# Kernel optimization log

Hardware: AMD Instinct MI355X
Metric: run time of the kernel (lower is better)

The kernel has to match this reference:

```python
import math
import jax, jax.numpy as jnp
import numpy as np

NUM_HEADS = 32

def _alibi_slopes(n: int) -> jnp.ndarray:
    cp2 = 2 ** int(math.floor(math.log2(n)))
    base = 2.0 ** (-(2.0 ** (-(math.log2(cp2) - 3))))
    slopes = base ** np.arange(1, cp2 + 1, dtype=np.float64)
    if cp2 != n:
        extra_base = 2.0 ** (-(2.0 ** (-(math.log2(2 * cp2) - 3))))
        rem = min(cp2, n - cp2)
        slopes = np.concatenate([slopes, extra_base ** np.arange(1, 1 + 2 * rem, 2, dtype=np.float64)])
    return jnp.asarray(slopes, dtype=jnp.float32)


def setup_inputs() -> dict:
    key = jax.random.key(0)
    k1, k2, k3 = jax.random.split(key, 3)
    B, S, E, H, D = 2, 2048, 4096, NUM_HEADS, 128
    hidden_states = jax.random.normal(k1, (B, S, E), dtype=jnp.float32)
    # torch Linear y = x @ W^T; we store transposed weights [in, out]
    w_qkv = jax.random.normal(k2, (E, H * D + 2 * D), dtype=jnp.float32) * 0.02
    w_c = jax.random.normal(k3, (E, E), dtype=jnp.float32) * 0.02
    return {"hidden_states": hidden_states, "w_qkv": w_qkv, "w_c": w_c}


def reference(hidden_states, w_qkv, w_c):
    B, S, E = hidden_states.shape
    H = NUM_HEADS
    D = E // H
    scaling = D ** -0.5

    qkv = hidden_states @ w_qkv                      # [B,S,H*D+2D]
    q = qkv[..., : H * D].reshape(B, S, H, D)        # [B,S,H,D]
    k = qkv[..., H * D: H * D + D]                   # [B,S,D] single KV head (MQA)
    v = qkv[..., H * D + D:]                         # [B,S,D]

    pos = jnp.arange(S)
    slopes = _alibi_slopes(H)                        # [H]
    # ALiBi: slope * (k_pos - q_pos), <= 0 in the causal region
    bias = slopes[:, None, None] * (pos[None, None, :] - pos[None, :, None]).astype(jnp.float32)  # [H,S,S]

    scores = jnp.einsum('bqhd,bkd->bhqk', q, k) * scaling + bias[None]  # [B,H,S,S]
    causal = pos[:, None] >= pos[None, :]            # [S,S]
    scores = jnp.where(causal[None, None], scores, jnp.finfo(scores.dtype).min)
    probs = jax.nn.softmax(scores, axis=-1)
    attn = jnp.einsum('bhqk,bkd->bqhd', probs, v).reshape(B, S, E)
    return attn @ w_c
```

## Files before the change

kernel.cpp:

```cpp
#include <hip/hip_runtime.h>
#include <hip/hip_bf16.h>

typedef unsigned short u16;
typedef unsigned int u32;
typedef __attribute__((ext_vector_type(8))) short s16x8;
typedef __attribute__((ext_vector_type(4))) float f32x4;

#define MFMA_BF16(a, b, c) __builtin_amdgcn_mfma_f32_16x16x32_bf16(a, b, c, 0, 0, 0)

__device__ __forceinline__ u16 f2bf(float f) {
  union { float f; u32 u; } c; c.f = f;
  return (u16)((c.u + 0x7FFFu + ((c.u >> 16) & 1u)) >> 16);
}

__device__ __forceinline__ u32 pkbf(float a, float b) {
  float2 t; t.x = a; t.y = b;
  __hip_bfloat162 h = __float22bfloat162_rn(t);
  union { __hip_bfloat162 h; u32 u; } c; c.h = h; return c.u;
}

__device__ __forceinline__ void gll16(const void* g, void* l) {
  __builtin_amdgcn_global_load_lds((const __attribute__((address_space(1))) void*)g,
                                   (__attribute__((address_space(3))) void*)l, 16, 0, 0);
}

__device__ __forceinline__ f32x4 f4zero() { f32x4 z = {0.f, 0.f, 0.f, 0.f}; return z; }

__global__ void cvt_bf16_kernel(const float4* __restrict__ in, u16* __restrict__ out, int n4) {
  int i = blockIdx.x * 256 + threadIdx.x;
  if (i >= n4) return;
  float4 v = in[i];
  uint2 w;
  w.x = (u32)f2bf(v.x) | ((u32)f2bf(v.y) << 16);
  w.y = (u32)f2bf(v.z) | ((u32)f2bf(v.w) << 16);
  *reinterpret_cast<uint2*>(out + (size_t)i * 4) = w;
}

__global__ void transpose_cvt_kernel(const float* __restrict__ in, u16* __restrict__ out,
                                     int R, int C) {
  __shared__ float tile[32][33];
  int tx = threadIdx.x, ty = threadIdx.y;
  int r0 = blockIdx.y * 32, c0 = blockIdx.x * 32;
#pragma unroll
  for (int i = 0; i < 32; i += 8)
    tile[ty + i][tx] = in[(size_t)(r0 + ty + i) * C + c0 + tx];
  __syncthreads();
#pragma unroll
  for (int i = 0; i < 32; i += 8)
    out[(size_t)(c0 + ty + i) * R + r0 + tx] = f2bf(tile[tx][ty + i]);
}


#define BARRIER __builtin_amdgcn_s_barrier()
#define LGKM0 asm volatile("s_waitcnt lgkmcnt(0)" ::: "memory")
#define PRIO1 __builtin_amdgcn_s_setprio(1)
#define PRIO0 __builtin_amdgcn_s_setprio(0)
#define VM4 asm volatile("s_waitcnt vmcnt(4)" ::: "memory")
#define VM0 asm volatile("s_waitcnt vmcnt(0)" ::: "memory")
#define NOPSTMT do {} while (0)

#define RD_A(dst, PR, QM) do { _Pragma("unroll")                                         \
  for (int mi2 = 0; mi2 < 4; ++mi2) {                                                    \
    dst[mi2][0] = *(const s16x8*)(smem + (PR)*32768 + (QM)*16384 + mi2*2048 + aOff0);    \
    dst[mi2][1] = *(const s16x8*)(smem + (PR)*32768 + (QM)*16384 + mi2*2048 + aOff1);    \
  } } while (0)

#define RD_B(dst, PR, QN) do { _Pragma("unroll")                                         \
  for (int ni2 = 0; ni2 < 2; ++ni2) {                                                    \
    dst[ni2][0] = *(const s16x8*)(smem + 65536 + (PR)*32768 + (QN)*16384 + ni2*2048 + bOff0); \
    dst[ni2][1] = *(const s16x8*)(smem + 65536 + (PR)*32768 + (QN)*16384 + ni2*2048 + bOff1); \
  } } while (0)

#define MFMA_Q(QM, QN, Af, Bf) do { _Pragma("unroll")                                    \
  for (int ks = 0; ks < 2; ++ks) { _Pragma("unroll")                                     \
    for (int mi2 = 0; mi2 < 4; ++mi2) { _Pragma("unroll")                                \
      for (int ni2 = 0; ni2 < 2; ++ni2)                                                  \
        acc[(QM)*4+mi2][(QN)*2+ni2] =                                                    \
            MFMA_BF16(Af[mi2][ks], Bf[ni2][ks], acc[(QM)*4+mi2][(QN)*2+ni2]);            \
  } } } while (0)

#define STAGE_PAIR(x, PW, kn) do {                                                       \
  gll16(srcA[x] + (kn), smem + (PW)*32768 + (x)*8192 + tt*16);                           \
  gll16(srcB[x] + (kn), smem + 65536 + (PW)*32768 + (x)*8192 + tt*16);                   \
} while (0)

#define STAGE_H1(PW, kn) do { STAGE_PAIR(0, PW, kn); STAGE_PAIR(1, PW, kn); } while (0)
#define STAGE_H2(PW, kn) do { STAGE_PAIR(2, PW, kn); STAGE_PAIR(3, PW, kn); } while (0)

#define TILE_BODY(PR, ST1, ST2, W1, W4) do {                                             \
  s16x8 a0[4][2], a1[4][2], b0[2][2], b1[2][2];                                          \
                       \
  RD_A(a0, PR, 0); RD_B(b0, PR, 0);                                                      \
  ST1;                                                                                   \
  BARRIER; LGKM0; PRIO1; MFMA_Q(0, 0, a0, b0); PRIO0;                                    \
  W1; BARRIER;                                                                           \
                            \
  RD_B(b1, PR, 1);                                                                       \
  ST2;                                                                                   \
  BARRIER; LGKM0; PRIO1; MFMA_Q(0, 1, a0, b1); PRIO0; BARRIER;                           \
                                                    \
  RD_A(a1, PR, 1);                                                                       \
  BARRIER; LGKM0; PRIO1; MFMA_Q(1, 1, a1, b1); PRIO0; BARRIER;                           \
                                                 \
  RD_B(b0, PR, 0);                                                                       \
  BARRIER; LGKM0; PRIO1; MFMA_Q(1, 0, a1, b0); PRIO0;                                    \
  W4; BARRIER;                                                                           \
} while (0)

#define TILE_MAIN(PR, PW, kn) TILE_BODY(PR, STAGE_H1(PW, kn), STAGE_H2(PW, kn), VM4, VM4)
#define TILE_LAST(PR) TILE_BODY(PR, NOPSTMT, NOPSTMT, VM0, NOPSTMT)

template<int EPI>
__global__ __launch_bounds__(512, 2)
void gemm256_kernel(const u16* __restrict__ A, const u16* __restrict__ Bt,
                    float* __restrict__ Cf, u16* __restrict__ Cq,
                    u16* __restrict__ Ck, u16* __restrict__ Cvt,
                    int N, int K) {
  __shared__ __align__(16) char smem[131072];
  const int tt = threadIdx.x;
  const int w = tt >> 6, l = tt & 63;
  const int li = l & 15, g = l >> 4;
  const int wm = w >> 2, wn = w & 3;

  const int gx = gridDim.x;
  const int nwg = gx * gridDim.y;
  int id = blockIdx.y * gx + blockIdx.x;
  id = (id & 7) * (nwg >> 3) + (id >> 3);
  const int bn = id % gx, bm = id / gx;

  f32x4 acc[8][4];
#pragma unroll
  for (int i = 0; i < 8; ++i)
#pragma unroll
    for (int j = 0; j < 4; ++j) acc[i][j] = f4zero();

  const int q8 = (((tt & 7) ^ ((tt >> 3) & 7)) * 8);
  const u16* srcA[4];
  const u16* srcB[4];
#pragma unroll
  for (int x = 0; x < 4; ++x) {
    const int arow = (x & 1) * 128 + (x >> 1) * 64 + (tt >> 3);
    srcA[x] = A + (size_t)(bm * 256 + arow) * K + q8;
    const int rho = x * 64 + (tt >> 3);
    const int qn_ = rho >> 7, rem = rho & 127;
    const int wn_ = rem >> 5, rr = rem & 31;
    const int brow = wn_ * 64 + qn_ * 32 + rr;
    srcB[x] = Bt + (size_t)(bn * 256 + brow) * K + q8;
  }

  const int gr0 = (g ^ (li & 7)) * 16;
  const int aOff0 = wm * 8192 + li * 128 + gr0;
  const int aOff1 = aOff0 ^ 64;
  const int bOff0 = wn * 4096 + li * 128 + gr0;
  const int bOff1 = bOff0 ^ 64;

  STAGE_H1(0, 0);
  STAGE_H2(0, 0);
  VM0;
  BARRIER;

  for (int t2 = 0; t2 < 62; t2 += 2) {
    TILE_MAIN(0, 1, (t2 + 1) * 64);
    TILE_MAIN(1, 0, (t2 + 2) * 64);
  }
  TILE_MAIN(0, 1, 63 * 64);
  TILE_LAST(1);

#pragma unroll
  for (int mi = 0; mi < 8; ++mi) {
#pragma unroll
    for (int ni = 0; ni < 4; ++ni) {
      const int row0 = bm * 256 + wm * 128 + mi * 16 + g * 4;
      const int col = bn * 256 + wn * 64 + ni * 16 + li;
#pragma unroll
      for (int r = 0; r < 4; ++r) {
        const int m = row0 + r;
        const float v = acc[mi][ni][r];
        if (EPI == 0) {
          Cf[(size_t)m * N + col] = v;
        } else {
          const int bb2 = m >> 11, s = m & 2047;
          const int kt = s >> 5;
          const size_t tb = (size_t)(bb2 * 64 + kt);
          if (col < 4096) {
            Cq[(size_t)m * 4096 + col] = f2bf(v);
          } else if (col < 4224) {
            const int d = col - 4096, kr = s & 31;
            const int mk = kr >> 4, lii = kr & 15;
            const int kk = d >> 5, gg = (d >> 3) & 3, e = d & 7;
            Ck[(tb * 8 + mk * 4 + kk) * 512 + (gg * 16 + lii) * 8 + e] = f2bf(v);
          } else {
            const int d = col - 4224, kp = s & 31;
            const int mf = d >> 4, lii = d & 15;
            const int gg = kp >> 3, e = kp & 7;
            Cvt[(tb * 8 + mf) * 512 + (gg * 16 + lii) * 8 + e] = f2bf(v);
          }
        }
      }
    }
  }
}


__device__ __forceinline__ void load_ktile(s16x8 (&dst)[8], const u16* kf, size_t tb, int l) {
#pragma unroll
  for (int f = 0; f < 8; ++f)
    dst[f] = *(const s16x8*)&kf[(tb * 8 + f) * 512 + l * 8];
}

template<bool DIAG>
__device__ __forceinline__ void attn_tile(
    int kt, const u16* kf, const u16* vf, size_t bb64, int l, int li, int g,
    s16x8 (&use)[8], s16x8 (&fill)[8], bool do_fill,
    const s16x8 (&bq)[2][4], f32x4 (&acc)[8][2],
    float (&m_)[2], float (&lp)[2], float (&bias)[2],
    float c1, const float (&cjr)[8], float bstep, u16 (*Pw)[40]) {
  const size_t tb = bb64 + kt;
  s16x8 vr[8];
#pragma unroll
  for (int f = 0; f < 8; ++f)
    vr[f] = *(const s16x8*)&vf[(tb * 8 + f) * 512 + l * 8];
  if (do_fill) load_ktile(fill, kf, tb - 1, l);

  f32x4 sc[2][2];
  sc[0][0] = f4zero(); sc[0][1] = f4zero(); sc[1][0] = f4zero(); sc[1][1] = f4zero();
#pragma unroll
  for (int kk = 0; kk < 4; ++kk)
#pragma unroll
    for (int mk = 0; mk < 2; ++mk) {
      sc[mk][0] = MFMA_BF16(use[mk * 4 + kk], bq[0][kk], sc[mk][0]);
      sc[mk][1] = MFMA_BF16(use[mk * 4 + kk], bq[1][kk], sc[mk][1]);
    }

#pragma unroll
  for (int nq = 0; nq < 2; ++nq) {
    float sv[8];
    float pm = -3e38f;
    if (DIAG) {
#pragma unroll
      for (int mk = 0; mk < 2; ++mk)
#pragma unroll
        for (int r = 0; r < 4; ++r) {
          const int kd = mk * 16 + g * 4 + r - (nq * 16 + li);
          float s = fmaf(sc[mk][nq][r], c1, bias[nq] + cjr[mk * 4 + r]);
          s = (kd <= 0) ? s : -1e30f;
          sv[mk * 4 + r] = s;
          pm = fmaxf(pm, s);
        }
      pm = fmaxf(pm, __shfl_xor(pm, 16));
      pm = fmaxf(pm, __shfl_xor(pm, 32));
      m_[nq] = pm;
    } else {
#pragma unroll
      for (int mk = 0; mk < 2; ++mk)
#pragma unroll
        for (int r = 0; r < 4; ++r) {
          float s = fmaf(sc[mk][nq][r], c1, bias[nq] + cjr[mk * 4 + r]);
          sv[mk * 4 + r] = s;
          pm = fmaxf(pm, s);
        }
      if (__any(pm > m_[nq])) {
        pm = fmaxf(pm, __shfl_xor(pm, 16));
        pm = fmaxf(pm, __shfl_xor(pm, 32));
        const float nm = fmaxf(m_[nq], pm);
        const float scale = exp2f(m_[nq] - nm);
#pragma unroll
        for (int mf = 0; mf < 8; ++mf) acc[mf][nq] *= scale;
        lp[nq] *= scale;
        m_[nq] = nm;
      }
    }
    const float mref = m_[nq];
    float e[8];
#pragma unroll
    for (int j = 0; j < 8; ++j) e[j] = exp2f(sv[j] - mref);
    lp[nq] += ((e[0] + e[1]) + (e[2] + e[3])) + ((e[4] + e[5]) + (e[6] + e[7]));
#pragma unroll
    for (int mk = 0; mk < 2; ++mk) {
      uint2 wv;
      wv.x = pkbf(e[mk * 4 + 0], e[mk * 4 + 1]);
      wv.y = pkbf(e[mk * 4 + 2], e[mk * 4 + 3]);
      *reinterpret_cast<uint2*>(&Pw[nq * 16 + li][mk * 16 + g * 4]) = wv;
    }
    bias[nq] -= bstep;
  }

  s16x8 pb0 = *(const s16x8*)&Pw[li][g * 8];
  s16x8 pb1 = *(const s16x8*)&Pw[16 + li][g * 8];
#pragma unroll
  for (int mf = 0; mf < 8; ++mf) {
    acc[mf][0] = MFMA_BF16(vr[mf], pb0, acc[mf][0]);
    acc[mf][1] = MFMA_BF16(vr[mf], pb1, acc[mf][1]);
  }
}

__device__ __forceinline__ void attn_qtile(
    int qt, int h, int b, const u16* qbuf, const u16* kf, const u16* vf,
    u16* obuf, int l, int li, int g, float c1, float sl2, u16 (*Pw)[40]) {
  const int S = 2048;
  const int q0 = qt * 32;
  const size_t bb64 = (size_t)b * 64;

  s16x8 bq[2][4];
#pragma unroll
  for (int nq = 0; nq < 2; ++nq)
#pragma unroll
    for (int kk = 0; kk < 4; ++kk)
      bq[nq][kk] = *(const s16x8*)&qbuf[(size_t)(b * S + q0 + nq * 16 + li) * 4096
                                        + h * 128 + kk * 32 + g * 8];

  f32x4 acc[8][2];
#pragma unroll
  for (int mf = 0; mf < 8; ++mf) { acc[mf][0] = f4zero(); acc[mf][1] = f4zero(); }
  float m_[2] = {-3e38f, -3e38f};
  float lp[2] = {0.f, 0.f};

  float cjr[8];
#pragma unroll
  for (int j = 0; j < 8; ++j) cjr[j] = sl2 * (float)((j >> 2) * 16 + (j & 3));
  float bias[2];
#pragma unroll
  for (int nq = 0; nq < 2; ++nq)
    bias[nq] = sl2 * (float)(g * 4 - nq * 16 - li);
  const float bstep = sl2 * 32.f;

  s16x8 kA[8], kB[8];
  load_ktile(kA, kf, bb64 + qt, l);
  attn_tile<true>(qt, kf, vf, bb64, l, li, g, kA, kB, qt >= 1,
                  bq, acc, m_, lp, bias, c1, cjr, bstep, Pw);
  int kt = qt - 1;
  while (kt >= 1) {
    attn_tile<false>(kt, kf, vf, bb64, l, li, g, kB, kA, true,
                     bq, acc, m_, lp, bias, c1, cjr, bstep, Pw);
    attn_tile<false>(kt - 1, kf, vf, bb64, l, li, g, kA, kB, kt >= 2,
                     bq, acc, m_, lp, bias, c1, cjr, bstep, Pw);
    kt -= 2;
  }
  if (kt == 0)
    attn_tile<false>(0, kf, vf, bb64, l, li, g, kB, kA, false,
                     bq, acc, m_, lp, bias, c1, cjr, bstep, Pw);

#pragma unroll
  for (int nq = 0; nq < 2; ++nq) {
    float ls = lp[nq];
    ls += __shfl_xor(ls, 16);
    ls += __shfl_xor(ls, 32);
    const float inv = 1.f / ls;
    const size_t rowbase = (size_t)(b * S + q0 + nq * 16 + li) * 4096 + h * 128;
#pragma unroll
    for (int mf = 0; mf < 8; ++mf) {
      f32x4 v = acc[mf][nq];
      uint2 wv;
      wv.x = pkbf(v[0] * inv, v[1] * inv);
      wv.y = pkbf(v[2] * inv, v[3] * inv);
      *reinterpret_cast<uint2*>(&obuf[rowbase + mf * 16 + g * 4]) = wv;
    }
  }
}

__global__ __launch_bounds__(64, 2)
void attn_kernel(const u16* __restrict__ qbuf, const u16* __restrict__ kf,
                 const u16* __restrict__ vf, u16* __restrict__ obuf) {
  const int p = blockIdx.x, h = blockIdx.y, b = blockIdx.z;
  const int l = threadIdx.x, li = l & 15, g = l >> 4;
  const float L2E = 1.4426950408889634f;
  const float slope = exp2f(-0.25f * (float)(h + 1));
  const float c1 = 0.08838834764831845f * L2E;
  const float sl2 = slope * L2E;
  __shared__ __align__(16) u16 P[32][40];
  attn_qtile(63 - p, h, b, qbuf, kf, vf, obuf, l, li, g, c1, sl2, P);
  attn_qtile(p, h, b, qbuf, kf, vf, obuf, l, li, g, c1, sl2, P);
}

extern "C" void kernel_launch(void* const* d_in, const int* in_sizes, int n_in,
                              void* d_out, int out_size, void* d_ws, size_t ws_size,
                              hipStream_t stream) {
  (void)in_sizes; (void)n_in; (void)out_size; (void)ws_size;
  const float* hidden = (const float*)d_in[0];
  const float* w_qkv = (const float*)d_in[1];
  const float* w_c = (const float*)d_in[2];
  float* out = (float*)d_out;
  char* ws = (char*)d_ws;

  u16* hid_bf = (u16*)(ws + 0);
  u16* wT     = (u16*)(ws + 33554432);
  u16* qbuf   = (u16*)(ws + 69206016);
  u16* kbuf   = (u16*)(ws + 102760448);
  u16* vtbuf  = (u16*)(ws + 103809024);

  cvt_bf16_kernel<<<16384, 256, 0, stream>>>((const float4*)hidden, hid_bf, 4194304);
  transpose_cvt_kernel<<<dim3(136, 128), dim3(32, 8), 0, stream>>>(w_qkv, wT, 4096, 4352);
  gemm256_kernel<1><<<dim3(17, 16), 512, 0, stream>>>(hid_bf, wT, nullptr, qbuf, kbuf, vtbuf,
                                                      4352, 4096);
  attn_kernel<<<dim3(32, 32, 2), 64, 0, stream>>>(qbuf, kbuf, vtbuf, hid_bf);
  transpose_cvt_kernel<<<dim3(128, 128), dim3(32, 8), 0, stream>>>(w_c, wT, 4096, 4096);
  gemm256_kernel<0><<<dim3(16, 16), 512, 0, stream>>>(hid_bf, wT, out, nullptr, nullptr, nullptr,
                                                      4096, 4096);
}
```

Before: 503.9 us.

## Fold K/V projection columns into Q-GEMM tiles instead of separate tile column

```diff
diff --git a/kernel.cpp b/kernel.cpp
--- a/kernel.cpp
+++ b/kernel.cpp
@@ -55,9 +55,12 @@
 #define LGKM0 asm volatile("s_waitcnt lgkmcnt(0)" ::: "memory")
 #define PRIO1 __builtin_amdgcn_s_setprio(1)
 #define PRIO0 __builtin_amdgcn_s_setprio(0)
+#define VM6 asm volatile("s_waitcnt vmcnt(6)" ::: "memory")
 #define VM4 asm volatile("s_waitcnt vmcnt(4)" ::: "memory")
+#define VM2 asm volatile("s_waitcnt vmcnt(2)" ::: "memory")
 #define VM0 asm volatile("s_waitcnt vmcnt(0)" ::: "memory")
 #define NOPSTMT do {} while (0)
+#define W1EPI do { if constexpr (EPI == 1) { VM6; } else { VM2; } } while (0)
 
 #define RD_A(dst, PR, QM) do { _Pragma("unroll")                                         \
   for (int mi2 = 0; mi2 < 4; ++mi2) {                                                    \
@@ -84,31 +87,49 @@
   gll16(srcB[x] + (kn), smem + 65536 + (PW)*32768 + (x)*8192 + tt*16);                   \
 } while (0)
 
-#define STAGE_H1(PW, kn) do { STAGE_PAIR(0, PW, kn); STAGE_PAIR(1, PW, kn); } while (0)
-#define STAGE_H2(PW, kn) do { STAGE_PAIR(2, PW, kn); STAGE_PAIR(3, PW, kn); } while (0)
-
-#define TILE_BODY(PR, ST1, ST2, W1, W4) do {                                             \
+#define TILE_BODY(PR, KB, S1, S2, S3, S4, W1, W4) do {                                   \
   s16x8 a0[4][2], a1[4][2], b0[2][2], b1[2][2];                                          \
-                       \
+  s16x8 bkv[2][2]; s16x8 sa[2];                                                          \
+                                                                           \
   RD_A(a0, PR, 0); RD_B(b0, PR, 0);                                                      \
-  ST1;                                                                                   \
+  if constexpr (EPI == 1) {                                                              \
+    const u16* kvp = Bt + (size_t)(4096 + w * 32 + li) * K + (KB) + g * 8;               \
+    bkv[0][0] = *(const s16x8*)(kvp);                                                    \
+    bkv[0][1] = *(const s16x8*)(kvp + 32);                                               \
+    bkv[1][0] = *(const s16x8*)(kvp + (size_t)16 * K);                                   \
+    bkv[1][1] = *(const s16x8*)(kvp + (size_t)16 * K + 32);                              \
+  }                                                                                      \
+  S1;                                                                                    \
   BARRIER; LGKM0; PRIO1; MFMA_Q(0, 0, a0, b0); PRIO0;                                    \
   W1; BARRIER;                                                                           \
-                            \
+                                                                           \
   RD_B(b1, PR, 1);                                                                       \
-  ST2;                                                                                   \
+  S2;                                                                                    \
   BARRIER; LGKM0; PRIO1; MFMA_Q(0, 1, a0, b1); PRIO0; BARRIER;                           \
-                                                    \
+                                                                           \
   RD_A(a1, PR, 1);                                                                       \
+  S3;                                                                                    \
   BARRIER; LGKM0; PRIO1; MFMA_Q(1, 1, a1, b1); PRIO0; BARRIER;                           \
-                                                 \
+                                                                \
   RD_B(b0, PR, 0);                                                                       \
-  BARRIER; LGKM0; PRIO1; MFMA_Q(1, 0, a1, b0); PRIO0;                                    \
-  W4; BARRIER;                                                                           \
+  if constexpr (EPI == 1) {                                                              \
+    sa[0] = *(const s16x8*)(smem + (PR)*32768 + aKV);                                    \
+    sa[1] = *(const s16x8*)(smem + (PR)*32768 + (aKV ^ 64));                             \
+  }                                                                                      \
+  S4;                                                                                    \
+  BARRIER; LGKM0; PRIO1; MFMA_Q(1, 0, a1, b0);                                           \
+  if constexpr (EPI == 1) { _Pragma("unroll")                                            \
+    for (int ks2 = 0; ks2 < 2; ++ks2) { _Pragma("unroll")                                \
+      for (int cs2 = 0; cs2 < 2; ++cs2)                                                  \
+        acc_kv[cs2] = MFMA_BF16(sa[ks2], bkv[cs2][ks2], acc_kv[cs2]);                    \
+  } }                                                                                    \
+  PRIO0; W4; BARRIER;                                                                    \
 } while (0)
 
-#define TILE_MAIN(PR, PW, kn) TILE_BODY(PR, STAGE_H1(PW, kn), STAGE_H2(PW, kn), VM4, VM4)
-#define TILE_LAST(PR) TILE_BODY(PR, NOPSTMT, NOPSTMT, VM0, NOPSTMT)
+#define TILE_MAIN(PR, PW, T) TILE_BODY(PR, (T)*64,                                       \
+  STAGE_PAIR(0, PW, ((T)+1)*64), STAGE_PAIR(1, PW, ((T)+1)*64),                          \
+  STAGE_PAIR(2, PW, ((T)+1)*64), STAGE_PAIR(3, PW, ((T)+1)*64), W1EPI, VM4)
+#define TILE_LAST(PR, T) TILE_BODY(PR, (T)*64, NOPSTMT, NOPSTMT, NOPSTMT, NOPSTMT, VM0, NOPSTMT)
 
 template<int EPI>
 __global__ __launch_bounds__(512, 2)
@@ -133,6 +154,8 @@
   for (int i = 0; i < 8; ++i)
 #pragma unroll
     for (int j = 0; j < 4; ++j) acc[i][j] = f4zero();
+  f32x4 acc_kv[2];
+  acc_kv[0] = f4zero(); acc_kv[1] = f4zero();
 
   const int q8 = (((tt & 7) ^ ((tt >> 3) & 7)) * 8);
   const u16* srcA[4];
@@ -153,18 +176,20 @@
   const int aOff1 = aOff0 ^ 64;
   const int bOff0 = wn * 4096 + li * 128 + gr0;
   const int bOff1 = bOff0 ^ 64;
-
-  STAGE_H1(0, 0);
-  STAGE_H2(0, 0);
+  const int aKV = ((bn >> 2) & 1) * 16384 + (bn >> 3) * 8192 + (bn & 3) * 2048
+                  + li * 128 + gr0;
+
+#pragma unroll
+  for (int x = 0; x < 4; ++x) STAGE_PAIR(x, 0, 0);
   VM0;
   BARRIER;
 
   for (int t2 = 0; t2 < 62; t2 += 2) {
-    TILE_MAIN(0, 1, (t2 + 1) * 64);
-    TILE_MAIN(1, 0, (t2 + 2) * 64);
-  }
-  TILE_MAIN(0, 1, 63 * 64);
-  TILE_LAST(1);
+    TILE_MAIN(0, 1, t2);
+    TILE_MAIN(1, 0, t2 + 1);
+  }
+  TILE_MAIN(0, 1, 62);
+  TILE_LAST(1, 63);
 
 #pragma unroll
   for (int mi = 0; mi < 8; ++mi) {
@@ -179,22 +204,32 @@
         if (EPI == 0) {
           Cf[(size_t)m * N + col] = v;
         } else {
-          const int bb2 = m >> 11, s = m & 2047;
-          const int kt = s >> 5;
-          const size_t tb = (size_t)(bb2 * 64 + kt);
-          if (col < 4096) {
-            Cq[(size_t)m * 4096 + col] = f2bf(v);
-          } else if (col < 4224) {
-            const int d = col - 4096, kr = s & 31;
-            const int mk = kr >> 4, lii = kr & 15;
-            const int kk = d >> 5, gg = (d >> 3) & 3, e = d & 7;
-            Ck[(tb * 8 + mk * 4 + kk) * 512 + (gg * 16 + lii) * 8 + e] = f2bf(v);
-          } else {
-            const int d = col - 4224, kp = s & 31;
-            const int mf = d >> 4, lii = d & 15;
-            const int gg = kp >> 3, e = kp & 7;
-            Cvt[(tb * 8 + mf) * 512 + (gg * 16 + lii) * 8 + e] = f2bf(v);
-          }
+          Cq[(size_t)m * 4096 + col] = f2bf(v);
+        }
+      }
+    }
+  }
+  if constexpr (EPI == 1) {
+#pragma unroll
+    for (int cs = 0; cs < 2; ++cs) {
+      const int col = 4096 + w * 32 + cs * 16 + li;
+#pragma unroll
+      for (int r = 0; r < 4; ++r) {
+        const int m = bm * 256 + bn * 16 + g * 4 + r;
+        const float v = acc_kv[cs][r];
+        const int bb2 = m >> 11, s = m & 2047;
+        const int kt = s >> 5;
+        const size_t tb = (size_t)(bb2 * 64 + kt);
+        if (col < 4224) {
+          const int d = col - 4096, kr = s & 31;
+          const int mk = kr >> 4, lii = kr & 15;
+          const int kk = d >> 5, gg = (d >> 3) & 3, e = d & 7;
+          Ck[(tb * 8 + mk * 4 + kk) * 512 + (gg * 16 + lii) * 8 + e] = f2bf(v);
+        } else {
+          const int d = col - 4224, kp = s & 31;
+          const int mf = d >> 4, lii = d & 15;
+          const int gg = kp >> 3, e = kp & 7;
+          Cvt[(tb * 8 + mf) * 512 + (gg * 16 + lii) * 8 + e] = f2bf(v);
         }
       }
     }
@@ -390,7 +425,7 @@
 
   cvt_bf16_kernel<<<16384, 256, 0, stream>>>((const float4*)hidden, hid_bf, 4194304);
   transpose_cvt_kernel<<<dim3(136, 128), dim3(32, 8), 0, stream>>>(w_qkv, wT, 4096, 4352);
-  gemm256_kernel<1><<<dim3(17, 16), 512, 0, stream>>>(hid_bf, wT, nullptr, qbuf, kbuf, vtbuf,
+  gemm256_kernel<1><<<dim3(16, 16), 512, 0, stream>>>(hid_bf, wT, nullptr, qbuf, kbuf, vtbuf,
                                                       4352, 4096);
   attn_kernel<<<dim3(32, 32, 2), 64, 0, stream>>>(qbuf, kbuf, vtbuf, hid_bf);
   transpose_cvt_kernel<<<dim3(128, 128), dim3(32, 8), 0, stream>>>(w_c, wT, 4096, 4096);
```

New measurement: 485.8 us. 3.6% less time.
